# Optimization experiments

Measured on AMD Instinct MI355X. Metric: run time of the kernel, lower is better.

Reference implementation:

```python
import jax, jax.numpy as jnp
import numpy as np

B, L, D = 4, 2048, 512
N_HEAD, D_K, D_V = 8, 64, 64
D_INNER, N_LAYERS, NUM_TYPES = 2048, 4, 22
PAD = 0
LN_EPS = 1e-6


def _layer_norm(x, g, b):
    m = jnp.mean(x, axis=-1, keepdims=True)
    v = jnp.mean((x - m) ** 2, axis=-1, keepdims=True)
    return (x - m) * jax.lax.rsqrt(v + LN_EPS) * g + b


def _temporal_enc(time, non_pad_mask):
    # position_vec[i] = 10000^(2*(i//2)/d_model)
    i = np.arange(D)
    pos_vec = jnp.asarray(10000.0 ** (2.0 * (i // 2) / D), dtype=jnp.float32)
    r = time[:, :, None] / pos_vec                      # [B,L,D]
    even = (jnp.arange(D) % 2) == 0
    r = jnp.where(even, jnp.sin(r), jnp.cos(r))
    return r * non_pad_mask


def setup_inputs() -> dict:
    key = jax.random.key(0)
    ks = jax.random.split(key, 20)
    event_type = jax.random.randint(ks[0], (B, L), 0, NUM_TYPES + 1)
    event_time = jnp.cumsum(jax.random.uniform(ks[1], (B, L), dtype=jnp.float32), axis=1)
    non_pad_mask = (event_type != PAD).astype(jnp.float32)[:, :, None]
    s = 0.02
    emb = jax.random.normal(ks[2], (NUM_TYPES + 1, D), dtype=jnp.float32) * s
    emb = emb.at[PAD].set(0.0)  # padding_idx row
    Wq = jax.random.normal(ks[3], (N_LAYERS, D, N_HEAD * D_K), dtype=jnp.float32) * s
    Wk = jax.random.normal(ks[4], (N_LAYERS, D, N_HEAD * D_K), dtype=jnp.float32) * s
    Wv = jax.random.normal(ks[5], (N_LAYERS, D, N_HEAD * D_V), dtype=jnp.float32) * s
    fc_w = jax.random.normal(ks[6], (N_LAYERS, N_HEAD * D_V, D), dtype=jnp.float32) * s
    fc_b = jnp.zeros((N_LAYERS, D), dtype=jnp.float32)
    ln1_g = jnp.ones((N_LAYERS, D), dtype=jnp.float32)
    ln1_b = jnp.zeros((N_LAYERS, D), dtype=jnp.float32)
    W1 = jax.random.normal(ks[7], (N_LAYERS, D, D_INNER), dtype=jnp.float32) * s
    b1 = jnp.zeros((N_LAYERS, D_INNER), dtype=jnp.float32)
    W2 = jax.random.normal(ks[8], (N_LAYERS, D_INNER, D), dtype=jnp.float32) * s
    b2 = jnp.zeros((N_LAYERS, D), dtype=jnp.float32)
    ln2_g = jnp.ones((N_LAYERS, D), dtype=jnp.float32)
    ln2_b = jnp.zeros((N_LAYERS, D), dtype=jnp.float32)
    return dict(event_type=event_type, event_time=event_time, non_pad_mask=non_pad_mask,
                emb=emb, Wq=Wq, Wk=Wk, Wv=Wv, fc_w=fc_w, fc_b=fc_b,
                ln1_g=ln1_g, ln1_b=ln1_b, W1=W1, b1=b1, W2=W2, b2=b2,
                ln2_g=ln2_g, ln2_b=ln2_b)


def reference(event_type, event_time, non_pad_mask, emb, Wq, Wk, Wv, fc_w, fc_b,
              ln1_g, ln1_b, W1, b1, W2, b2, ln2_g, ln2_b):
    # Attention mask. NOTE: in the source, slf_attn_mask_sparse is overwritten by
    # the keypad mask, so the effective mask is padding | causal.
    pad = (event_type == PAD)                                   # [B,L]
    keypad = pad[:, None, :]                                    # [B,1(L_q),L_k] broadcast
    subseq = jnp.triu(jnp.ones((L, L), dtype=bool), k=1)        # [L,L]
    mask = (keypad | subseq)[:, None, :, :]                     # [B,1,L,L] over heads

    tem = _temporal_enc(event_time, non_pad_mask)               # [B,L,D]
    x = emb[event_type]                                         # [B,L,D]
    scale = 1.0 / jnp.sqrt(jnp.float32(D_K))

    for l in range(N_LAYERS):
        x = x + tem
        # --- multi-head attention (post-LN, THP style) ---
        residual = x
        q = (x @ Wq[l]).reshape(B, L, N_HEAD, D_K)
        k = (x @ Wk[l]).reshape(B, L, N_HEAD, D_K)
        v = (x @ Wv[l]).reshape(B, L, N_HEAD, D_V)
        scores = jnp.einsum('bqhd,bkhd->bhqk', q, k) * scale    # [B,H,L,L]
        scores = jnp.where(mask, -1e9, scores)
        attn = jax.nn.softmax(scores, axis=-1)
        out = jnp.einsum('bhqk,bkhd->bqhd', attn, v).reshape(B, L, N_HEAD * D_V)
        out = out @ fc_w[l] + fc_b[l] + residual
        x = _layer_norm(out, ln1_g[l], ln1_b[l])
        x = x * non_pad_mask
        # --- position-wise FFN (exact GELU, post-LN) ---
        residual = x
        h = jax.nn.gelu(x @ W1[l] + b1[l], approximate=False)
        y = h @ W2[l] + b2[l] + residual
        x = _layer_norm(y, ln2_g[l], ln2_b[l])
        x = x * non_pad_mask
    return x
```

## Files before the change

kernel.cpp:

```cpp
#include <hip/hip_runtime.h>
#include <math.h>

#define BB 4
#define LL 2048
#define DD 512
#define NH 8
#define DINNER 2048
#define NLAYERS 4
#define MM (BB * LL)

typedef __attribute__((ext_vector_type(8))) __bf16 bf16x8;
typedef __attribute__((ext_vector_type(4))) float f32x4;
typedef __attribute__((ext_vector_type(4))) unsigned short us4;

__device__ __forceinline__ unsigned short f2b(float f) {
  union { __bf16 h; unsigned short u; } v;
  v.h = (__bf16)f;
  return v.u;
}
__device__ __forceinline__ float b2f(unsigned short h) {
  union { unsigned u; float f; } v; v.u = ((unsigned)h) << 16; return v.f;
}
__device__ __forceinline__ unsigned pk2(float lo, float hi) {
  return (unsigned)f2b(lo) | ((unsigned)f2b(hi) << 16);
}
__device__ __forceinline__ float exp2f_fast(float x) {
  float r; asm("v_exp_f32 %0, %1" : "=v"(r) : "v"(x)); return r;
}

__device__ __forceinline__ void gload16(const void* g, void* l) {
  __builtin_amdgcn_global_load_lds(
      (const __attribute__((address_space(1))) void*)g,
      (__attribute__((address_space(3))) void*)l, 16, 0, 0);
}

__global__ __launch_bounds__(512) void init_kernel(
    const int* __restrict__ etype, const float* __restrict__ etime,
    const float* __restrict__ npm, const float* __restrict__ emb,
    float* __restrict__ tem, float* __restrict__ xa,
    unsigned short* __restrict__ xab) {
  int row = blockIdx.x;
  int d = threadIdx.x;
  float t = etime[row];
  float mask = npm[row];
  int dd = d & ~1;
  float pv = expf(9.210340371976184f * ((float)dd * (1.0f / (float)DD)));
  float r = t / pv;
  float val = (d & 1) ? cosf(r) : sinf(r);
  float tv = val * mask;
  tem[(size_t)row * DD + d] = tv;
  int ty = etype[row];
  float a = emb[(size_t)ty * DD + d] + tv;
  xa[(size_t)row * DD + d] = a;
  xab[(size_t)row * DD + d] = f2b(a);
}

__global__ __launch_bounds__(256) void wtrans_kernel(
    const float* __restrict__ in, unsigned short* __restrict__ out,
    int K, int N, long in_ls, long out_ls) {
  __shared__ float t[32][33];
  int l = blockIdx.z;
  int n0 = blockIdx.x * 32, k0 = blockIdx.y * 32;
  int tx = threadIdx.x & 31, ty = threadIdx.x >> 5;
  const float* ip = in + (size_t)l * in_ls;
  unsigned short* op = out + (size_t)l * out_ls;
#pragma unroll
  for (int r = ty; r < 32; r += 8)
    t[r][tx] = ip[(size_t)(k0 + r) * N + n0 + tx];
  __syncthreads();
#pragma unroll
  for (int r = ty; r < 32; r += 8)
    op[(size_t)(n0 + r) * K + k0 + tx] = f2b(t[tx][r]);
}

template <int BM, bool BIAS, bool RES, bool GELU_, bool OBF16>
__global__ __launch_bounds__(256) void gemm_kernel(
    const unsigned short* __restrict__ A, const unsigned short* __restrict__ WT,
    const float* __restrict__ bias, const float* __restrict__ res, int ldres,
    void* __restrict__ Cv, int ldc, int M, int N, int K) {
  __shared__ unsigned short As[2][BM * 32];
  __shared__ unsigned short Bs[2][128 * 32];
  constexpr int NT = (BM == 128) ? 4 : 2;
  int tid = threadIdx.x;
  int w = tid >> 6, l = tid & 63;
  int li = l & 15, g = l >> 4;
  int row0 = blockIdx.y * BM, col0 = blockIdx.x * 128;
  int wm = (BM == 128) ? (w & 1) * 64 : 0;
  int wnb = (BM == 128) ? (w >> 1) * 64 : w * 32;
  f32x4 acc[4][NT];
#pragma unroll
  for (int i = 0; i < 4; i++)
#pragma unroll
    for (int j = 0; j < NT; j++) acc[i][j] = (f32x4){0.f, 0.f, 0.f, 0.f};

  int lr = l >> 2;
  int lc = (l & 3) ^ (lr & 3);

  auto stage = [&](int bb, int kb) {
    int k0 = kb * 32;
    if (BM == 128) {
#pragma unroll
      for (int i = 0; i < 2; i++) {
        int ai = w * 2 + i;
        gload16(A + (size_t)(row0 + ai * 16 + lr) * K + k0 + lc * 8,
                &As[bb][ai * 512]);
        gload16(WT + (size_t)(col0 + ai * 16 + lr) * K + k0 + lc * 8,
                &Bs[bb][ai * 512]);
      }
    } else {
      gload16(A + (size_t)(row0 + w * 16 + lr) * K + k0 + lc * 8,
              &As[bb][w * 512]);
#pragma unroll
      for (int i = 0; i < 2; i++) {
        int bi = w * 2 + i;
        gload16(WT + (size_t)(col0 + bi * 16 + lr) * K + k0 + lc * 8,
                &Bs[bb][bi * 512]);
      }
    }
  };

  int nk = K >> 5;
  stage(0, 0);
  __syncthreads();
  int buf = 0;
  for (int kb = 0; kb < nk; kb++) {
    if (kb + 1 < nk) stage(buf ^ 1, kb + 1);
    bf16x8 af[4], bf_[NT];
#pragma unroll
    for (int mt = 0; mt < 4; mt++) {
      int r = wm + mt * 16 + li;
      af[mt] = *(const bf16x8*)&As[buf][r * 32 + ((g ^ (r & 3)) * 8)];
    }
#pragma unroll
    for (int nt = 0; nt < NT; nt++) {
      int r = wnb + nt * 16 + li;
      bf_[nt] = *(const bf16x8*)&Bs[buf][r * 32 + ((g ^ (r & 3)) * 8)];
    }
#pragma unroll
    for (int mt = 0; mt < 4; mt++)
#pragma unroll
      for (int nt = 0; nt < NT; nt++)
        acc[mt][nt] = __builtin_amdgcn_mfma_f32_16x16x32_bf16(
            af[mt], bf_[nt], acc[mt][nt], 0, 0, 0);
    __syncthreads();
    buf ^= 1;
  }
#pragma unroll
  for (int mt = 0; mt < 4; mt++) {
#pragma unroll
    for (int nt = 0; nt < NT; nt++) {
#pragma unroll
      for (int r = 0; r < 4; r++) {
        int row = row0 + wm + mt * 16 + g * 4 + r;
        int col = col0 + wnb + nt * 16 + li;
        float v = acc[mt][nt][r];
        if (BIAS) v += bias[col];
        if (RES) v += res[(size_t)row * ldres + col];
        if (GELU_) v = 0.5f * v * (1.0f + erff(v * 0.70710678118654752f));
        if (OBF16)
          ((unsigned short*)Cv)[(size_t)row * ldc + col] = f2b(v);
        else
          ((float*)Cv)[(size_t)row * ldc + col] = v;
      }
    }
  }
}

__global__ __launch_bounds__(256) void vtrans_kernel(
    const unsigned short* __restrict__ qkv, unsigned short* __restrict__ vT) {
  __shared__ unsigned short t[64][65];
  int bh = blockIdx.y;
  int b = bh >> 3, h = bh & 7;
  int l0 = blockIdx.x * 64;
  int tid = threadIdx.x;
  int c = tid & 63, p = tid >> 6;
#pragma unroll
  for (int r = p; r < 64; r += 4)
    t[r][c] = qkv[(size_t)(b * LL + l0 + r) * 1536 + 1024 + h * 64 + c];
  __syncthreads();
#pragma unroll
  for (int r = p; r < 64; r += 4)
    vT[((size_t)bh * 64 + r) * LL + l0 + c] = t[c][r];
}

__global__ __launch_bounds__(256) void meanv_kernel(
    const unsigned short* __restrict__ vT, float* __restrict__ meanV) {
  __shared__ float red[256];
  int bh = blockIdx.x;
  int tid = threadIdx.x;
  int d = tid >> 2, p = tid & 3;
  const unsigned short* vp = vT + ((size_t)bh * 64 + d) * LL;
  float s = 0.f;
  for (int i = p * 512; i < p * 512 + 512; i++) s += b2f(vp[i]);
  red[tid] = s;
  __syncthreads();
  if (p == 0)
    meanV[bh * 64 + d] =
        (red[tid] + red[tid + 1] + red[tid + 2] + red[tid + 3]) *
        (1.0f / (float)LL);
}

__global__ __launch_bounds__(256) void attn_kernel(
    const unsigned short* __restrict__ qkv, const unsigned short* __restrict__ vT,
    const int* __restrict__ etype, unsigned short* __restrict__ opart,
    float* __restrict__ ml) {
  __shared__ unsigned short Ks[2][64 * 64];
  __shared__ unsigned short Ps[64][72];
  int hwbid = blockIdx.x;
  int work = (hwbid & 7) * 256 + (hwbid >> 3);
  int bh = work >> 6;
  int rem = work & 63;
  int qt = 31 - (rem >> 1);
  int half = rem & 1;
  int h = bh & 7, b = bh >> 3;
  int q0 = qt * 64;
  int nt = qt + 1;
  int ha = (nt + 1) >> 1;
  int j0 = half ? ha : 0;
  int j1 = half ? nt : ha;
  int pidx = (bh * 32 + qt) * 2 + half;
  int tid = threadIdx.x, w = tid >> 6, l = tid & 63;
  int g = l >> 4, li = l & 15;
  const float SC = 0.125f * 1.44269504f;

  f32x4 o[4];
#pragma unroll
  for (int n = 0; n < 4; n++) o[n] = (f32x4){0.f, 0.f, 0.f, 0.f};
  float mreg[4], lreg[4];
#pragma unroll
  for (int r = 0; r < 4; r++) { mreg[r] = -3.0e38f; lreg[r] = 0.f; }

  if (j0 < j1) {
    const unsigned short* qrp =
        qkv + (size_t)(b * LL + q0 + w * 16 + li) * 1536 + h * 64;
    bf16x8 aq0 = *(const bf16x8*)&qrp[g * 8];
    bf16x8 aq1 = *(const bf16x8*)&qrp[32 + g * 8];

#pragma unroll
    for (int e = 0; e < 2; e++) {
      int idx = e * 256 + tid;
      int r = idx >> 3;
      int src = (l & 7) ^ (r & 7);
      gload16(
          qkv + (size_t)(b * LL + j0 * 64 + r) * 1536 + 512 + h * 64 + src * 8,
          &Ks[0][(e * 256 + w * 64) * 8]);
    }
    __syncthreads();

    int cur = 0;
    for (int j = j0; j < j1; j++) {
      int k0 = j << 6;
      if (j + 1 < j1) {
#pragma unroll
        for (int e = 0; e < 2; e++) {
          int idx = e * 256 + tid;
          int r = idx >> 3;
          int src = (l & 7) ^ (r & 7);
          gload16(qkv + (size_t)(b * LL + k0 + 64 + r) * 1536 + 512 + h * 64 +
                      src * 8,
                  &Ks[cur ^ 1][(e * 256 + w * 64) * 8]);
        }
      }
      bf16x8 bv0[4], bv1[4];
      float pb[4];
#pragma unroll
      for (int n = 0; n < 4; n++) {
        const unsigned short* vp =
            vT + ((size_t)(bh * 64 + n * 16 + li)) * LL + k0;
        bv0[n] = *(const bf16x8*)&vp[g * 8];
        bv1[n] = *(const bf16x8*)&vp[32 + g * 8];
        pb[n] = (etype[b * LL + k0 + n * 16 + li] == 0) ? -1.0e9f : 0.f;
      }
      f32x4 s[4];
#pragma unroll
      for (int n = 0; n < 4; n++) {
        int rK = n * 16 + li;
        const unsigned short* kb = &Ks[cur][rK * 64];
        bf16x8 bk0 = *(const bf16x8*)&kb[(g ^ (rK & 7)) * 8];
        bf16x8 bk1 = *(const bf16x8*)&kb[((g + 4) ^ (rK & 7)) * 8];
        f32x4 a = (f32x4){0.f, 0.f, 0.f, 0.f};
        __builtin_amdgcn_s_setprio(1);
        a = __builtin_amdgcn_mfma_f32_16x16x32_bf16(aq0, bk0, a, 0, 0, 0);
        a = __builtin_amdgcn_mfma_f32_16x16x32_bf16(aq1, bk1, a, 0, 0, 0);
        __builtin_amdgcn_s_setprio(0);
        s[n] = a;
      }
      if (j == qt) {
#pragma unroll
        for (int n = 0; n < 4; n++) {
          int key = k0 + n * 16 + li;
#pragma unroll
          for (int r = 0; r < 4; r++) {
            int qrow = q0 + w * 16 + g * 4 + r;
            float sv = fmaf(s[n][r], SC, pb[n]);
            if (key > qrow) sv = -1.0e9f;
            s[n][r] = sv;
          }
        }
      } else {
#pragma unroll
        for (int n = 0; n < 4; n++)
#pragma unroll
          for (int r = 0; r < 4; r++) s[n][r] = fmaf(s[n][r], SC, pb[n]);
      }
      float pm[4], corr[4], psum[4];
#pragma unroll
      for (int r = 0; r < 4; r++)
        pm[r] = fmaxf(fmaxf(s[0][r], s[1][r]), fmaxf(s[2][r], s[3][r]));
#pragma unroll
      for (int msk = 1; msk <= 8; msk <<= 1)
#pragma unroll
        for (int r = 0; r < 4; r++)
          pm[r] = fmaxf(pm[r], __shfl_xor(pm[r], msk, 64));
#pragma unroll
      for (int r = 0; r < 4; r++) {
        float mnew = fmaxf(mreg[r], pm[r]);
        corr[r] = exp2f_fast(mreg[r] - mnew);
        mreg[r] = mnew;
        float ps = 0.f;
#pragma unroll
        for (int n = 0; n < 4; n++) {
          float p = exp2f_fast(s[n][r] - mnew);
          s[n][r] = p;
          ps += p;
        }
        psum[r] = ps;
      }
#pragma unroll
      for (int msk = 1; msk <= 8; msk <<= 1)
#pragma unroll
        for (int r = 0; r < 4; r++) psum[r] += __shfl_xor(psum[r], msk, 64);
#pragma unroll
      for (int r = 0; r < 4; r++) lreg[r] = lreg[r] * corr[r] + psum[r];
#pragma unroll
      for (int n = 0; n < 4; n++)
#pragma unroll
        for (int r = 0; r < 4; r++)
          Ps[w * 16 + g * 4 + r][n * 16 + li] = f2b(s[n][r]);
#pragma unroll
      for (int n = 0; n < 4; n++)
#pragma unroll
        for (int r = 0; r < 4; r++) o[n][r] *= corr[r];
      bf16x8 ap0 = *(const bf16x8*)&Ps[w * 16 + li][g * 8];
      bf16x8 ap1 = *(const bf16x8*)&Ps[w * 16 + li][32 + g * 8];
      __builtin_amdgcn_s_setprio(1);
#pragma unroll
      for (int n = 0; n < 4; n++) {
        o[n] = __builtin_amdgcn_mfma_f32_16x16x32_bf16(ap0, bv0[n], o[n], 0, 0, 0);
        o[n] = __builtin_amdgcn_mfma_f32_16x16x32_bf16(ap1, bv1[n], o[n], 0, 0, 0);
      }
      __builtin_amdgcn_s_setprio(0);
      __syncthreads();
      cur ^= 1;
    }
  }
#pragma unroll
  for (int r = 0; r < 4; r++) {
    int qrl = w * 16 + g * 4 + r;
    float inv = (lreg[r] > 0.f) ? 1.0f / lreg[r] : 0.f;
#pragma unroll
    for (int n = 0; n < 4; n++)
      opart[((size_t)pidx * 64 + qrl) * 64 + n * 16 + li] = f2b(o[n][r] * inv);
    if (li == 0) {
      ml[(size_t)pidx * 128 + qrl] = mreg[r];
      ml[(size_t)pidx * 128 + 64 + qrl] = lreg[r];
    }
  }
}

__global__ __launch_bounds__(256) void amerge_kernel(
    const unsigned short* __restrict__ opart, const float* __restrict__ ml,
    const float* __restrict__ meanV, unsigned short* __restrict__ ao) {
  int blk = blockIdx.x;
  int bh = blk >> 5, qt = blk & 31;
  int b = bh >> 3, h = bh & 7;
  int tid = threadIdx.x;
  int d = tid & 63;
  int pA = blk * 2, pB = blk * 2 + 1;
  for (int rr = tid >> 6; rr < 64; rr += 4) {
    float mA = ml[(size_t)pA * 128 + rr], lA = ml[(size_t)pA * 128 + 64 + rr];
    float mB = ml[(size_t)pB * 128 + rr], lB = ml[(size_t)pB * 128 + 64 + rr];
    float m = fmaxf(mA, mB);
    float v;
    if (m <= -1.0e8f) {
      v = meanV[bh * 64 + d];
    } else {
      float acc = 0.f, wsum = 0.f;
      if (lA > 0.f) {
        float wA = exp2f_fast(mA - m) * lA;
        acc += b2f(opart[((size_t)pA * 64 + rr) * 64 + d]) * wA;
        wsum += wA;
      }
      if (lB > 0.f) {
        float wB = exp2f_fast(mB - m) * lB;
        acc += b2f(opart[((size_t)pB * 64 + rr) * 64 + d]) * wB;
        wsum += wB;
      }
      v = acc / wsum;
    }
    int qr = qt * 64 + rr;
    ao[(size_t)(b * LL + qr) * DD + h * 64 + d] = f2b(v);
  }
}

template <bool ADDTEM>
__global__ __launch_bounds__(256) void ln_kernel(
    const unsigned short* __restrict__ in, const float* __restrict__ g,
    const float* __restrict__ bta, const float* __restrict__ npm,
    const float* __restrict__ tem, float* __restrict__ out,
    float* __restrict__ out2, unsigned short* __restrict__ out_bf) {
  __shared__ float red[4];
  int row = blockIdx.x;
  int tid = threadIdx.x;
  unsigned u = ((const unsigned*)(in + (size_t)row * DD))[tid];
  float v0 = b2f((unsigned short)u), v1 = b2f((unsigned short)(u >> 16));
  int e0 = tid * 2, e1 = tid * 2 + 1;
  float s = v0 + v1;
#pragma unroll
  for (int o = 32; o > 0; o >>= 1) s += __shfl_down(s, o, 64);
  if ((tid & 63) == 0) red[tid >> 6] = s;
  __syncthreads();
  float mean = (red[0] + red[1] + red[2] + red[3]) * (1.0f / (float)DD);
  float d0 = v0 - mean, d1 = v1 - mean;
  float sq = d0 * d0 + d1 * d1;
#pragma unroll
  for (int o = 32; o > 0; o >>= 1) sq += __shfl_down(sq, o, 64);
  __syncthreads();
  if ((tid & 63) == 0) red[tid >> 6] = sq;
  __syncthreads();
  float var = (red[0] + red[1] + red[2] + red[3]) * (1.0f / (float)DD);
  float rstd = rsqrtf(var + 1e-6f);
  float m = npm[row];
  float o0 = (d0 * rstd * g[e0] + bta[e0]) * m;
  float o1 = (d1 * rstd * g[e1] + bta[e1]) * m;
  ((float2*)(out + (size_t)row * DD))[tid] = make_float2(o0, o1);
  if (ADDTEM) {
    float2 tv = ((const float2*)(tem + (size_t)row * DD))[tid];
    float a0 = o0 + tv.x, a1 = o1 + tv.y;
    ((float2*)(out2 + (size_t)row * DD))[tid] = make_float2(a0, a1);
    ((unsigned*)(out_bf + (size_t)row * DD))[tid] = pk2(a0, a1);
  } else {
    ((unsigned*)(out_bf + (size_t)row * DD))[tid] = pk2(o0, o1);
  }
}

extern "C" void kernel_launch(void* const* d_in, const int* in_sizes, int n_in,
                              void* d_out, int out_size, void* d_ws,
                              size_t ws_size, hipStream_t stream) {
  const int* etype = (const int*)d_in[0];
  const float* etime = (const float*)d_in[1];
  const float* npm = (const float*)d_in[2];
  const float* emb = (const float*)d_in[3];
  const float* Wq = (const float*)d_in[4];
  const float* Wk = (const float*)d_in[5];
  const float* Wv = (const float*)d_in[6];
  const float* fc_w = (const float*)d_in[7];
  const float* fc_b = (const float*)d_in[8];
  const float* ln1_g = (const float*)d_in[9];
  const float* ln1_b = (const float*)d_in[10];
  const float* W1 = (const float*)d_in[11];
  const float* b1 = (const float*)d_in[12];
  const float* W2 = (const float*)d_in[13];
  const float* b2 = (const float*)d_in[14];
  const float* ln2_g = (const float*)d_in[15];
  const float* ln2_b = (const float*)d_in[16];

  float* x = (float*)d_out;
  char* ws = (char*)d_ws;
  const size_t SZF = (size_t)MM * DD * sizeof(float);
  const size_t SZB = (size_t)MM * DD * sizeof(short);
  float* tem = (float*)ws; ws += SZF;
  float* xa  = (float*)ws; ws += SZF;
  unsigned short* xab = (unsigned short*)ws; ws += SZB;
  unsigned short* xbf = (unsigned short*)ws; ws += SZB;
  unsigned short* qkv = (unsigned short*)ws; ws += (size_t)MM * 1536 * 2;
  unsigned short* vT  = (unsigned short*)ws; ws += (size_t)BB * NH * 64 * LL * 2;
  unsigned short* ao  = (unsigned short*)ws; ws += SZB;
  unsigned short* hb  = (unsigned short*)ws; ws += (size_t)MM * DINNER * 2;
  unsigned short* ybb = (unsigned short*)ws; ws += SZB;
  unsigned short* qkvT = (unsigned short*)ws; ws += (size_t)NLAYERS * 1536 * 512 * 2;
  unsigned short* fcT  = (unsigned short*)ws; ws += (size_t)NLAYERS * 512 * 512 * 2;
  unsigned short* W1T  = (unsigned short*)ws; ws += (size_t)NLAYERS * 2048 * 512 * 2;
  unsigned short* W2T  = (unsigned short*)ws; ws += (size_t)NLAYERS * 512 * 2048 * 2;
  float* meanV = (float*)ws; ws += BB * NH * 64 * sizeof(float);
  unsigned short* opart = (unsigned short*)ws; ws += (size_t)2048 * 64 * 64 * 2;
  float* ml = (float*)ws; ws += (size_t)2048 * 128 * sizeof(float);

  init_kernel<<<MM, 512, 0, stream>>>(etype, etime, npm, emb, tem, xa, xab);

  wtrans_kernel<<<dim3(16, 16, NLAYERS), 256, 0, stream>>>(
      Wq, qkvT + 0 * 512 * 512, 512, 512, 512L * 512, 1536L * 512);
  wtrans_kernel<<<dim3(16, 16, NLAYERS), 256, 0, stream>>>(
      Wk, qkvT + 1 * 512 * 512, 512, 512, 512L * 512, 1536L * 512);
  wtrans_kernel<<<dim3(16, 16, NLAYERS), 256, 0, stream>>>(
      Wv, qkvT + 2 * 512 * 512, 512, 512, 512L * 512, 1536L * 512);
  wtrans_kernel<<<dim3(16, 16, NLAYERS), 256, 0, stream>>>(
      fc_w, fcT, 512, 512, 512L * 512, 512L * 512);
  wtrans_kernel<<<dim3(64, 16, NLAYERS), 256, 0, stream>>>(
      W1, W1T, 512, 2048, 512L * 2048, 2048L * 512);
  wtrans_kernel<<<dim3(16, 64, NLAYERS), 256, 0, stream>>>(
      W2, W2T, 2048, 512, 2048L * 512, 512L * 2048);

  for (int l = 0; l < NLAYERS; l++) {
    gemm_kernel<128, false, false, false, true><<<dim3(12, 64), 256, 0, stream>>>(
        xab, qkvT + (size_t)l * 1536 * 512, nullptr, nullptr, 0, qkv, 1536,
        MM, 1536, 512);

    vtrans_kernel<<<dim3(32, 32), 256, 0, stream>>>(qkv, vT);
    meanv_kernel<<<BB * NH, 256, 0, stream>>>(vT, meanV);
    attn_kernel<<<2048, 256, 0, stream>>>(qkv, vT, etype, opart, ml);
    amerge_kernel<<<1024, 256, 0, stream>>>(opart, ml, meanV, ao);

    gemm_kernel<64, true, true, false, true><<<dim3(4, 128), 256, 0, stream>>>(
        ao, fcT + (size_t)l * 512 * 512, fc_b + (size_t)l * 512, xa, 512, ybb,
        512, MM, 512, 512);
    ln_kernel<false><<<MM, 256, 0, stream>>>(
        ybb, ln1_g + (size_t)l * 512, ln1_b + (size_t)l * 512, npm, nullptr, x,
        nullptr, xbf);

    gemm_kernel<128, true, false, true, true><<<dim3(16, 64), 256, 0, stream>>>(
        xbf, W1T + (size_t)l * 2048 * 512, b1 + (size_t)l * 2048, nullptr, 0,
        hb, 2048, MM, 2048, 512);
    gemm_kernel<64, true, true, false, true><<<dim3(4, 128), 256, 0, stream>>>(
        hb, W2T + (size_t)l * 512 * 2048, b2 + (size_t)l * 512, x, 512, ybb,
        512, MM, 512, 2048);
    ln_kernel<true><<<MM, 256, 0, stream>>>(
        ybb, ln2_g + (size_t)l * 512, ln2_b + (size_t)l * 512, npm, tem, x, xa,
        xab);
  }
}
```

Measured before the change: 1.059 ms.

## Process two adjacent query tiles per attention block to share K/V loads

```diff
diff --git a/kernel.cpp b/kernel.cpp
--- a/kernel.cpp
+++ b/kernel.cpp
@@ -207,163 +207,239 @@
   __shared__ unsigned short Ks[2][64 * 64];
   __shared__ unsigned short Ps[64][72];
   int hwbid = blockIdx.x;
-  int work = (hwbid & 7) * 256 + (hwbid >> 3);
-  int bh = work >> 6;
-  int rem = work & 63;
-  int qt = 31 - (rem >> 1);
+  int work = (hwbid & 7) * 128 + (hwbid >> 3);
+  int bh = work >> 5;
+  int rem = work & 31;
+  int t = 15 - (rem >> 1);
   int half = rem & 1;
   int h = bh & 7, b = bh >> 3;
-  int q0 = qt * 64;
-  int nt = qt + 1;
-  int ha = (nt + 1) >> 1;
+  int qt1 = 2 * t, qt2 = 2 * t + 1;
+  int q01 = qt1 * 64, q02 = qt2 * 64;
+  int nt = 2 * t + 2;
+  int ha = t + 1;
   int j0 = half ? ha : 0;
   int j1 = half ? nt : ha;
-  int pidx = (bh * 32 + qt) * 2 + half;
+  int pidx1 = (bh * 32 + qt1) * 2 + half;
+  int pidx2 = (bh * 32 + qt2) * 2 + half;
   int tid = threadIdx.x, w = tid >> 6, l = tid & 63;
   int g = l >> 4, li = l & 15;
   const float SC = 0.125f * 1.44269504f;
 
-  f32x4 o[4];
-#pragma unroll
-  for (int n = 0; n < 4; n++) o[n] = (f32x4){0.f, 0.f, 0.f, 0.f};
-  float mreg[4], lreg[4];
-#pragma unroll
-  for (int r = 0; r < 4; r++) { mreg[r] = -3.0e38f; lreg[r] = 0.f; }
-
-  if (j0 < j1) {
-    const unsigned short* qrp =
-        qkv + (size_t)(b * LL + q0 + w * 16 + li) * 1536 + h * 64;
-    bf16x8 aq0 = *(const bf16x8*)&qrp[g * 8];
-    bf16x8 aq1 = *(const bf16x8*)&qrp[32 + g * 8];
-
-#pragma unroll
-    for (int e = 0; e < 2; e++) {
-      int idx = e * 256 + tid;
-      int r = idx >> 3;
-      int src = (l & 7) ^ (r & 7);
-      gload16(
-          qkv + (size_t)(b * LL + j0 * 64 + r) * 1536 + 512 + h * 64 + src * 8,
-          &Ks[0][(e * 256 + w * 64) * 8]);
-    }
-    __syncthreads();
-
-    int cur = 0;
-    for (int j = j0; j < j1; j++) {
-      int k0 = j << 6;
-      if (j + 1 < j1) {
-#pragma unroll
-        for (int e = 0; e < 2; e++) {
-          int idx = e * 256 + tid;
-          int r = idx >> 3;
-          int src = (l & 7) ^ (r & 7);
-          gload16(qkv + (size_t)(b * LL + k0 + 64 + r) * 1536 + 512 + h * 64 +
-                      src * 8,
-                  &Ks[cur ^ 1][(e * 256 + w * 64) * 8]);
+  const unsigned short* qrp1 =
+      qkv + (size_t)(b * LL + q01 + w * 16 + li) * 1536 + h * 64;
+  const unsigned short* qrp2 =
+      qkv + (size_t)(b * LL + q02 + w * 16 + li) * 1536 + h * 64;
+  bf16x8 aq10 = *(const bf16x8*)&qrp1[g * 8];
+  bf16x8 aq11 = *(const bf16x8*)&qrp1[32 + g * 8];
+  bf16x8 aq20 = *(const bf16x8*)&qrp2[g * 8];
+  bf16x8 aq21 = *(const bf16x8*)&qrp2[32 + g * 8];
+
+  f32x4 o1[4], o2[4];
+#pragma unroll
+  for (int n = 0; n < 4; n++) {
+    o1[n] = (f32x4){0.f, 0.f, 0.f, 0.f};
+    o2[n] = (f32x4){0.f, 0.f, 0.f, 0.f};
+  }
+  float m1[4], l1[4], m2[4], l2[4];
+#pragma unroll
+  for (int r = 0; r < 4; r++) {
+    m1[r] = -3.0e38f; l1[r] = 0.f;
+    m2[r] = -3.0e38f; l2[r] = 0.f;
+  }
+
+#pragma unroll
+  for (int e = 0; e < 2; e++) {
+    int idx = e * 256 + tid;
+    int r = idx >> 3;
+    int src = (l & 7) ^ (r & 7);
+    gload16(
+        qkv + (size_t)(b * LL + j0 * 64 + r) * 1536 + 512 + h * 64 + src * 8,
+        &Ks[0][(e * 256 + w * 64) * 8]);
+  }
+  __syncthreads();
+
+  int cur = 0;
+  for (int j = j0; j < j1; j++) {
+    int k0 = j << 6;
+    if (j + 1 < j1) {
+#pragma unroll
+      for (int e = 0; e < 2; e++) {
+        int idx = e * 256 + tid;
+        int r = idx >> 3;
+        int src = (l & 7) ^ (r & 7);
+        gload16(qkv + (size_t)(b * LL + k0 + 64 + r) * 1536 + 512 + h * 64 +
+                    src * 8,
+                &Ks[cur ^ 1][(e * 256 + w * 64) * 8]);
+      }
+    }
+    bf16x8 bv0[4], bv1[4];
+    float pb[4];
+#pragma unroll
+    for (int n = 0; n < 4; n++) {
+      const unsigned short* vp =
+          vT + ((size_t)(bh * 64 + n * 16 + li)) * LL + k0;
+      bv0[n] = *(const bf16x8*)&vp[g * 8];
+      bv1[n] = *(const bf16x8*)&vp[32 + g * 8];
+      pb[n] = (etype[b * LL + k0 + n * 16 + li] == 0) ? -1.0e9f : 0.f;
+    }
+    f32x4 s1[4], s2[4];
+#pragma unroll
+    for (int n = 0; n < 4; n++) {
+      int rK = n * 16 + li;
+      const unsigned short* kb = &Ks[cur][rK * 64];
+      bf16x8 bk0 = *(const bf16x8*)&kb[(g ^ (rK & 7)) * 8];
+      bf16x8 bk1 = *(const bf16x8*)&kb[((g + 4) ^ (rK & 7)) * 8];
+      __builtin_amdgcn_s_setprio(1);
+      f32x4 a1 = (f32x4){0.f, 0.f, 0.f, 0.f};
+      a1 = __builtin_amdgcn_mfma_f32_16x16x32_bf16(aq10, bk0, a1, 0, 0, 0);
+      a1 = __builtin_amdgcn_mfma_f32_16x16x32_bf16(aq11, bk1, a1, 0, 0, 0);
+      f32x4 a2 = (f32x4){0.f, 0.f, 0.f, 0.f};
+      a2 = __builtin_amdgcn_mfma_f32_16x16x32_bf16(aq20, bk0, a2, 0, 0, 0);
+      a2 = __builtin_amdgcn_mfma_f32_16x16x32_bf16(aq21, bk1, a2, 0, 0, 0);
+      __builtin_amdgcn_s_setprio(0);
+      s1[n] = a1;
+      s2[n] = a2;
+    }
+    if (j >= qt1) {
+#pragma unroll
+      for (int n = 0; n < 4; n++) {
+        int key = k0 + n * 16 + li;
+#pragma unroll
+        for (int r = 0; r < 4; r++) {
+          int qrow = q01 + w * 16 + g * 4 + r;
+          float sv = fmaf(s1[n][r], SC, pb[n]);
+          if (key > qrow) sv = -1.0e9f;
+          s1[n][r] = sv;
         }
       }
-      bf16x8 bv0[4], bv1[4];
-      float pb[4];
+    } else {
+#pragma unroll
+      for (int n = 0; n < 4; n++)
+#pragma unroll
+        for (int r = 0; r < 4; r++) s1[n][r] = fmaf(s1[n][r], SC, pb[n]);
+    }
+    if (j >= qt2) {
 #pragma unroll
       for (int n = 0; n < 4; n++) {
-        const unsigned short* vp =
-            vT + ((size_t)(bh * 64 + n * 16 + li)) * LL + k0;
-        bv0[n] = *(const bf16x8*)&vp[g * 8];
-        bv1[n] = *(const bf16x8*)&vp[32 + g * 8];
-        pb[n] = (etype[b * LL + k0 + n * 16 + li] == 0) ? -1.0e9f : 0.f;
-      }
-      f32x4 s[4];
+        int key = k0 + n * 16 + li;
+#pragma unroll
+        for (int r = 0; r < 4; r++) {
+          int qrow = q02 + w * 16 + g * 4 + r;
+          float sv = fmaf(s2[n][r], SC, pb[n]);
+          if (key > qrow) sv = -1.0e9f;
+          s2[n][r] = sv;
+        }
+      }
+    } else {
+#pragma unroll
+      for (int n = 0; n < 4; n++)
+#pragma unroll
+        for (int r = 0; r < 4; r++) s2[n][r] = fmaf(s2[n][r], SC, pb[n]);
+    }
+    float pm1[4], pm2[4], c1[4], c2[4], ps1[4], ps2[4];
+#pragma unroll
+    for (int r = 0; r < 4; r++) {
+      pm1[r] = fmaxf(fmaxf(s1[0][r], s1[1][r]), fmaxf(s1[2][r], s1[3][r]));
+      pm2[r] = fmaxf(fmaxf(s2[0][r], s2[1][r]), fmaxf(s2[2][r], s2[3][r]));
+    }
+#pragma unroll
+    for (int msk = 1; msk <= 8; msk <<= 1)
+#pragma unroll
+      for (int r = 0; r < 4; r++) {
+        pm1[r] = fmaxf(pm1[r], __shfl_xor(pm1[r], msk, 64));
+        pm2[r] = fmaxf(pm2[r], __shfl_xor(pm2[r], msk, 64));
+      }
+#pragma unroll
+    for (int r = 0; r < 4; r++) {
+      float mn1 = fmaxf(m1[r], pm1[r]);
+      float mn2 = fmaxf(m2[r], pm2[r]);
+      c1[r] = exp2f_fast(m1[r] - mn1);
+      c2[r] = exp2f_fast(m2[r] - mn2);
+      m1[r] = mn1;
+      m2[r] = mn2;
+      float a = 0.f, bsum = 0.f;
 #pragma unroll
       for (int n = 0; n < 4; n++) {
-        int rK = n * 16 + li;
-        const unsigned short* kb = &Ks[cur][rK * 64];
-        bf16x8 bk0 = *(const bf16x8*)&kb[(g ^ (rK & 7)) * 8];
-        bf16x8 bk1 = *(const bf16x8*)&kb[((g + 4) ^ (rK & 7)) * 8];
-        f32x4 a = (f32x4){0.f, 0.f, 0.f, 0.f};
-        __builtin_amdgcn_s_setprio(1);
-        a = __builtin_amdgcn_mfma_f32_16x16x32_bf16(aq0, bk0, a, 0, 0, 0);
-        a = __builtin_amdgcn_mfma_f32_16x16x32_bf16(aq1, bk1, a, 0, 0, 0);
-        __builtin_amdgcn_s_setprio(0);
-        s[n] = a;
-      }
-      if (j == qt) {
-#pragma unroll
-        for (int n = 0; n < 4; n++) {
-          int key = k0 + n * 16 + li;
-#pragma unroll
-          for (int r = 0; r < 4; r++) {
-            int qrow = q0 + w * 16 + g * 4 + r;
-            float sv = fmaf(s[n][r], SC, pb[n]);
-            if (key > qrow) sv = -1.0e9f;
-            s[n][r] = sv;
-          }
-        }
-      } else {
-#pragma unroll
-        for (int n = 0; n < 4; n++)
-#pragma unroll
-          for (int r = 0; r < 4; r++) s[n][r] = fmaf(s[n][r], SC, pb[n]);
-      }
-      float pm[4], corr[4], psum[4];
+        float p1 = exp2f_fast(s1[n][r] - mn1);
+        float p2 = exp2f_fast(s2[n][r] - mn2);
+        s1[n][r] = p1;
+        s2[n][r] = p2;
+        a += p1;
+        bsum += p2;
+      }
+      ps1[r] = a;
+      ps2[r] = bsum;
+    }
+#pragma unroll
+    for (int msk = 1; msk <= 8; msk <<= 1)
+#pragma unroll
+      for (int r = 0; r < 4; r++) {
+        ps1[r] += __shfl_xor(ps1[r], msk, 64);
+        ps2[r] += __shfl_xor(ps2[r], msk, 64);
+      }
+#pragma unroll
+    for (int r = 0; r < 4; r++) {
+      l1[r] = l1[r] * c1[r] + ps1[r];
+      l2[r] = l2[r] * c2[r] + ps2[r];
+    }
+#pragma unroll
+    for (int n = 0; n < 4; n++)
 #pragma unroll
       for (int r = 0; r < 4; r++)
-        pm[r] = fmaxf(fmaxf(s[0][r], s[1][r]), fmaxf(s[2][r], s[3][r]));
-#pragma unroll
-      for (int msk = 1; msk <= 8; msk <<= 1)
-#pragma unroll
-        for (int r = 0; r < 4; r++)
-          pm[r] = fmaxf(pm[r], __shfl_xor(pm[r], msk, 64));
-#pragma unroll
-      for (int r = 0; r < 4; r++) {
-        float mnew = fmaxf(mreg[r], pm[r]);
-        corr[r] = exp2f_fast(mreg[r] - mnew);
-        mreg[r] = mnew;
-        float ps = 0.f;
-#pragma unroll
-        for (int n = 0; n < 4; n++) {
-          float p = exp2f_fast(s[n][r] - mnew);
-          s[n][r] = p;
-          ps += p;
-        }
-        psum[r] = ps;
-      }
-#pragma unroll
-      for (int msk = 1; msk <= 8; msk <<= 1)
-#pragma unroll
-        for (int r = 0; r < 4; r++) psum[r] += __shfl_xor(psum[r], msk, 64);
-#pragma unroll
-      for (int r = 0; r < 4; r++) lreg[r] = lreg[r] * corr[r] + psum[r];
-#pragma unroll
-      for (int n = 0; n < 4; n++)
-#pragma unroll
-        for (int r = 0; r < 4; r++)
-          Ps[w * 16 + g * 4 + r][n * 16 + li] = f2b(s[n][r]);
-#pragma unroll
-      for (int n = 0; n < 4; n++)
-#pragma unroll
-        for (int r = 0; r < 4; r++) o[n][r] *= corr[r];
+        Ps[w * 16 + g * 4 + r][n * 16 + li] = f2b(s1[n][r]);
+#pragma unroll
+    for (int n = 0; n < 4; n++)
+#pragma unroll
+      for (int r = 0; r < 4; r++) o1[n][r] *= c1[r];
+    {
       bf16x8 ap0 = *(const bf16x8*)&Ps[w * 16 + li][g * 8];
       bf16x8 ap1 = *(const bf16x8*)&Ps[w * 16 + li][32 + g * 8];
       __builtin_amdgcn_s_setprio(1);
 #pragma unroll
       for (int n = 0; n < 4; n++) {
-        o[n] = __builtin_amdgcn_mfma_f32_16x16x32_bf16(ap0, bv0[n], o[n], 0, 0, 0);
-        o[n] = __builtin_amdgcn_mfma_f32_16x16x32_bf16(ap1, bv1[n], o[n], 0, 0, 0);
+        o1[n] = __builtin_amdgcn_mfma_f32_16x16x32_bf16(ap0, bv0[n], o1[n], 0, 0, 0);
+        o1[n] = __builtin_amdgcn_mfma_f32_16x16x32_bf16(ap1, bv1[n], o1[n], 0, 0, 0);
       }
       __builtin_amdgcn_s_setprio(0);
-      __syncthreads();
-      cur ^= 1;
-    }
+    }
+#pragma unroll
+    for (int n = 0; n < 4; n++)
+#pragma unroll
+      for (int r = 0; r < 4; r++)
+        Ps[w * 16 + g * 4 + r][n * 16 + li] = f2b(s2[n][r]);
+#pragma unroll
+    for (int n = 0; n < 4; n++)
+#pragma unroll
+      for (int r = 0; r < 4; r++) o2[n][r] *= c2[r];
+    {
+      bf16x8 ap0 = *(const bf16x8*)&Ps[w * 16 + li][g * 8];
+      bf16x8 ap1 = *(const bf16x8*)&Ps[w * 16 + li][32 + g * 8];
+      __builtin_amdgcn_s_setprio(1);
+#pragma unroll
+      for (int n = 0; n < 4; n++) {
+        o2[n] = __builtin_amdgcn_mfma_f32_16x16x32_bf16(ap0, bv0[n], o2[n], 0, 0, 0);
+        o2[n] = __builtin_amdgcn_mfma_f32_16x16x32_bf16(ap1, bv1[n], o2[n], 0, 0, 0);
+      }
+      __builtin_amdgcn_s_setprio(0);
+    }
+    __syncthreads();
+    cur ^= 1;
   }
 #pragma unroll
   for (int r = 0; r < 4; r++) {
     int qrl = w * 16 + g * 4 + r;
-    float inv = (lreg[r] > 0.f) ? 1.0f / lreg[r] : 0.f;
-#pragma unroll
-    for (int n = 0; n < 4; n++)
-      opart[((size_t)pidx * 64 + qrl) * 64 + n * 16 + li] = f2b(o[n][r] * inv);
+    float i1 = (l1[r] > 0.f) ? 1.0f / l1[r] : 0.f;
+    float i2 = (l2[r] > 0.f) ? 1.0f / l2[r] : 0.f;
+#pragma unroll
+    for (int n = 0; n < 4; n++) {
+      opart[((size_t)pidx1 * 64 + qrl) * 64 + n * 16 + li] = f2b(o1[n][r] * i1);
+      opart[((size_t)pidx2 * 64 + qrl) * 64 + n * 16 + li] = f2b(o2[n][r] * i2);
+    }
     if (li == 0) {
-      ml[(size_t)pidx * 128 + qrl] = mreg[r];
-      ml[(size_t)pidx * 128 + 64 + qrl] = lreg[r];
+      ml[(size_t)pidx1 * 128 + qrl] = m1[r];
+      ml[(size_t)pidx1 * 128 + 64 + qrl] = l1[r];
+      ml[(size_t)pidx2 * 128 + qrl] = m2[r];
+      ml[(size_t)pidx2 * 128 + 64 + qrl] = l2[r];
     }
   }
 }
@@ -508,7 +584,7 @@
 
     vtrans_kernel<<<dim3(32, 32), 256, 0, stream>>>(qkv, vT);
     meanv_kernel<<<BB * NH, 256, 0, stream>>>(vT, meanV);
-    attn_kernel<<<2048, 256, 0, stream>>>(qkv, vT, etype, opart, ml);
+    attn_kernel<<<1024, 256, 0, stream>>>(qkv, vT, etype, opart, ml);
     amerge_kernel<<<1024, 256, 0, stream>>>(opart, ml, meanV, ao);
 
     gemm_kernel<64, true, true, false, true><<<dim3(4, 128), 256, 0, stream>>>(
```

Measured after the change: 1.130 ms. 1.07x slower.
